# Optimization experiments

Measured on AMD Instinct MI355X. Metric: run time of the kernel, lower is better.

Reference implementation:

```python
import jax, jax.numpy as jnp
import numpy as np

GFD = 4096   # global feature dim (VGG fc7)
DH = 1024    # 2 * hidden_dim


def setup_inputs() -> dict:
    key = jax.random.key(0)
    ks = jax.random.split(key, 10)
    b, t_k = 32, 196
    s = lambda fan_in: 1.0 / np.sqrt(fan_in)
    return {
        "global_features": jax.random.normal(ks[0], (b, t_k, GFD), jnp.float32),
        "s_t_hat": jax.random.normal(ks[1], (b, DH), jnp.float32),
        "coverage_img": jnp.zeros((b, t_k, 1), jnp.float32),
        # params
        "Wg": jax.random.normal(ks[2], (GFD, GFD), jnp.float32) * s(GFD),
        "bg": jnp.zeros((GFD,), jnp.float32),
        "Gs": jax.random.normal(ks[3], (GFD, DH), jnp.float32) * s(GFD),
        "bgs": jnp.zeros((DH,), jnp.float32),
        "Wgs": jax.random.normal(ks[4], (DH, DH), jnp.float32) * s(DH),  # w_g_star, no bias
        "Wdec": jax.random.normal(ks[5], (DH, DH), jnp.float32) * s(DH),  # decode_proj
        "bdec": jnp.zeros((DH,), jnp.float32),
        "v": jax.random.normal(ks[6], (DH, 1), jnp.float32) * s(DH),  # score vector, no bias
    }


def reference(global_features, s_t_hat, coverage_img, Wg, bg, Gs, bgs, Wgs, Wdec, bdec, v):
    # g_star: project 4096-d region features -> 1024-d   [b, t_k, DH]
    g1 = global_features @ Wg + bg
    g_star = g1 @ Gs + bgs
    # additive (Bahdanau) scores with coverage
    w_g_star = g_star @ Wgs                       # [b, t_k, DH]
    dec_fea = s_t_hat @ Wdec + bdec               # [b, DH]
    e_a = jnp.tanh(w_g_star + dec_fea[:, None, :] + coverage_img)  # [b, t_k, DH]
    scores = e_a @ v                              # [b, t_k, 1]
    alpha_a = jax.nn.softmax(scores, axis=1)      # softmax over regions
    # attention-weighted context (the bmm)
    c_img = jnp.einsum("bt,btd->bd", alpha_a[..., 0], g_star)  # [b, DH]
    coverage_new = coverage_img + alpha_a
    return c_img, coverage_new, alpha_a
```

## Files before the change

### kernel.cpp

```cpp
#include <hip/hip_runtime.h>
#include <hip/hip_bf16.h>

typedef __attribute__((ext_vector_type(8))) short short8;
typedef __attribute__((ext_vector_type(4))) short short4v;
typedef __attribute__((ext_vector_type(4))) float floatx4;

#define GLOBAL_AS __attribute__((address_space(1)))
#define LDS_AS    __attribute__((address_space(3)))

__device__ __forceinline__ unsigned short f2bf_rne(float x) {
  unsigned int u = __float_as_uint(x);
  u += 0x7fffu + ((u >> 16) & 1u);
  return (unsigned short)(u >> 16);
}

__device__ __forceinline__ void cast8_body(const float* __restrict__ in,
                                           unsigned short* __restrict__ out,
                                           int blk, int n8) {
  int i = blk * 256 + threadIdx.x;
  if (i >= n8) return;
  const float4* p = (const float4*)in;
  float4 v0 = p[2 * i], v1 = p[2 * i + 1];
  short8 o;
  o[0] = (short)f2bf_rne(v0.x); o[1] = (short)f2bf_rne(v0.y);
  o[2] = (short)f2bf_rne(v0.z); o[3] = (short)f2bf_rne(v0.w);
  o[4] = (short)f2bf_rne(v1.x); o[5] = (short)f2bf_rne(v1.y);
  o[6] = (short)f2bf_rne(v1.z); o[7] = (short)f2bf_rne(v1.w);
  *(short8*)(out + 8 * (size_t)i) = o;
}

__device__ __forceinline__ void trans32_body(const float* __restrict__ in,
                                             unsigned short* __restrict__ out,
                                             int R, int C, int bx, int by) {
  __shared__ unsigned short tile[32][33];
  int tx = threadIdx.x & 31, ty = threadIdx.x >> 5;
  int r0 = by * 32, c0 = bx * 32;
#pragma unroll
  for (int j = 0; j < 32; j += 8)
    tile[ty + j][tx] = f2bf_rne(in[(size_t)(r0 + ty + j) * C + c0 + tx]);
  __syncthreads();
#pragma unroll
  for (int j = 0; j < 32; j += 8)
    out[(size_t)(c0 + ty + j) * R + r0 + tx] = tile[tx][ty + j];
}

__global__ void prep1_kernel(const float* __restrict__ gf, unsigned short* __restrict__ gf_bf,
                             const float* __restrict__ Wg, unsigned short* __restrict__ Wg_bf,
                             const float* __restrict__ Gs, unsigned short* __restrict__ GsT,
                             const float* __restrict__ bg, float* __restrict__ bias1,
                             const float* __restrict__ Wgs, unsigned short* __restrict__ WgsT,
                             const float* __restrict__ bdec, float* __restrict__ dec,
                             float* __restrict__ scores) {
  const int b = blockIdx.x;
  if (b < 12544) {
    cast8_body(gf, gf_bf, b, 3211264);
  } else if (b < 20736) {
    cast8_body(Wg, Wg_bf, b - 12544, 2097152);
  } else if (b < 24832) {
    int bb = b - 20736;
    trans32_body(Gs, GsT, 4096, 1024, bb & 31, bb >> 5);
  } else if (b < 24896) {
    int bb = b - 24832;
    int j = (bb & 3) * 256 + threadIdx.x;
    int k0 = (bb >> 2) * 256;
    float acc = 0.f;
    for (int k = 0; k < 256; ++k) acc += bg[k0 + k] * Gs[(size_t)(k0 + k) * 1024 + j];
    atomicAdd(&bias1[j], acc);
  } else if (b < 25920) {
    int bb = b - 24896;
    trans32_body(Wgs, WgsT, 1024, 1024, bb & 31, bb >> 5);
  } else if (b < 26048) {
    int i = (b - 25920) * 256 + threadIdx.x;
    dec[i] = bdec[i & 1023];
  } else {
    int i = (b - 26048) * 256 + threadIdx.x;
    if (i < 1568) ((float4*)scores)[i] = make_float4(0.f, 0.f, 0.f, 0.f);
  }
}

__global__ void dec_accum_kernel(const float* __restrict__ sth, const float* __restrict__ Wdec,
                                 float* __restrict__ dec) {
  __shared__ float ss[32][128];
  const int tid = threadIdx.x;
  const int k0 = blockIdx.y * 128;
  for (int i = tid; i < 32 * 128; i += 256) {
    int bb = i >> 7, kk = i & 127;
    ss[bb][kk] = sth[bb * 1024 + k0 + kk];
  }
  __syncthreads();
  const int j = blockIdx.x * 256 + tid;
  float acc[32];
#pragma unroll
  for (int b = 0; b < 32; ++b) acc[b] = 0.f;
  for (int kk = 0; kk < 128; ++kk) {
    float w = Wdec[(size_t)(k0 + kk) * 1024 + j];
#pragma unroll
    for (int b = 0; b < 32; ++b) acc[b] += ss[b][kk] * w;
  }
  for (int b = 0; b < 32; ++b) atomicAdd(&dec[b * 1024 + j], acc[b]);
}

__global__ __launch_bounds__(256) void reduce2_kernel(const float* __restrict__ p0,
                                                      const float* __restrict__ p1,
                                                      const float* __restrict__ bias,
                                                      float* __restrict__ gf32,
                                                      unsigned short* __restrict__ gb16) {
  const int i = blockIdx.x * 256 + threadIdx.x;
  float4 a = ((const float4*)p0)[i];
  float4 b = ((const float4*)p1)[i];
  float4 bv = ((const float4*)bias)[i & 255];
  float4 r;
  r.x = a.x + b.x + bv.x; r.y = a.y + b.y + bv.y;
  r.z = a.z + b.z + bv.z; r.w = a.w + b.w + bv.w;
  ((float4*)gf32)[i] = r;
  short4v o;
  o[0] = (short)f2bf_rne(r.x); o[1] = (short)f2bf_rne(r.y);
  o[2] = (short)f2bf_rne(r.z); o[3] = (short)f2bf_rne(r.w);
  *(short4v*)(gb16 + 4 * (size_t)i) = o;
}

template <int BM, int BN, bool WRITE_F32, bool WRITE_BF16, bool SWAPXY>
__global__ __launch_bounds__(256, 2) void gemm_tile_kernel(
    const unsigned short* __restrict__ A, const unsigned short* __restrict__ BT,
    float* __restrict__ Cf, unsigned short* __restrict__ Cb,
    int M, int N, int K, int Ksub, size_t csplit) {
  constexpr int AF = BM / 32;
  constexpr int BF = BN / 32;
  constexpr int ASLAB = BM * 64;
  constexpr int BSLAB = BN * 64;
  constexpr int ABUF = 2 * ASLAB;
  constexpr int BBUF = 2 * BSLAB;
  __shared__ unsigned short lds_a[BM * 128];
  __shared__ unsigned short lds_b[BN * 128];
  const int tid = threadIdx.x;
  const int lane = tid & 63;
  const int wave = tid >> 6;
  const int wm = wave >> 1, wn = wave & 1;
  const int quad = lane >> 4, col = lane & 15;

  const int gx = (int)gridDim.x;
  const int nwg = gx * (int)gridDim.y;
  const int bid = (int)blockIdx.y * gx + (int)blockIdx.x;
  const int swz = (bid & 7) * (nwg >> 3) + (bid >> 3);
  const int bx = swz % gx, by = swz / gx;
  const int m0 = (SWAPXY ? bx : by) * BM;
  const int n0 = (SWAPXY ? by : bx) * BN;
  const int kb = (int)blockIdx.z * Ksub;

  floatx4 acc[AF][BF] = {};

  const int srow = tid >> 2;
  const int skoff = (tid & 3) * 8;
  const unsigned short* a_ptr = A + (size_t)(m0 + srow) * K + kb + skoff;
  const unsigned short* b_ptr = BT + (size_t)(n0 + srow) * K + kb + skoff;
  const size_t rowskip = (size_t)64 * K;
  char* const la_dst = (char*)lds_a + tid * 16;
  char* const lb_dst = (char*)lds_b + tid * 16;

#pragma unroll
  for (int h = 0; h < BM / 64; ++h)
#pragma unroll
    for (int s = 0; s < 2; ++s)
      __builtin_amdgcn_global_load_lds((const GLOBAL_AS void*)(a_ptr + h * rowskip + s * 32),
                                       (LDS_AS void*)(la_dst + s * ASLAB + h * 4096), 16, 0, 0);
#pragma unroll
  for (int h = 0; h < BN / 64; ++h)
#pragma unroll
    for (int s = 0; s < 2; ++s)
      __builtin_amdgcn_global_load_lds((const GLOBAL_AS void*)(b_ptr + h * rowskip + s * 32),
                                       (LDS_AS void*)(lb_dst + s * BSLAB + h * 4096), 16, 0, 0);
  a_ptr += 64; b_ptr += 64;
  __syncthreads();

  const int NT = Ksub >> 6;
  int cur = 0;
  for (int t = 0; t < NT; ++t) {
    if (t + 1 < NT) {
      char* la = la_dst + (cur ^ 1) * ABUF;
      char* lb = lb_dst + (cur ^ 1) * BBUF;
#pragma unroll
      for (int h = 0; h < BM / 64; ++h)
#pragma unroll
        for (int s = 0; s < 2; ++s)
          __builtin_amdgcn_global_load_lds((const GLOBAL_AS void*)(a_ptr + h * rowskip + s * 32),
                                           (LDS_AS void*)(la + s * ASLAB + h * 4096), 16, 0, 0);
#pragma unroll
      for (int h = 0; h < BN / 64; ++h)
#pragma unroll
        for (int s = 0; s < 2; ++s)
          __builtin_amdgcn_global_load_lds((const GLOBAL_AS void*)(b_ptr + h * rowskip + s * 32),
                                           (LDS_AS void*)(lb + s * BSLAB + h * 4096), 16, 0, 0);
      a_ptr += 64; b_ptr += 64;
    }
    const char* pa = (const char*)lds_a + cur * ABUF;
    const char* pb = (const char*)lds_b + cur * BBUF;
#pragma unroll
    for (int s = 0; s < 2; ++s) {
      short8 af[AF], bf[BF];
#pragma unroll
      for (int tf = 0; tf < AF; ++tf)
        af[tf] = *(const short8*)(pa + s * ASLAB + (wm * (BM / 2) + tf * 16 + col) * 64 + quad * 16);
#pragma unroll
      for (int tf = 0; tf < BF; ++tf)
        bf[tf] = *(const short8*)(pb + s * BSLAB + (wn * (BN / 2) + tf * 16 + col) * 64 + quad * 16);
#pragma unroll
      for (int tm = 0; tm < AF; ++tm)
#pragma unroll
        for (int tn = 0; tn < BF; ++tn)
          acc[tm][tn] = __builtin_amdgcn_mfma_f32_16x16x32_bf16(af[tm], bf[tn], acc[tm][tn], 0, 0, 0);
    }
    __syncthreads();
    cur ^= 1;
  }

  float* Cfz = Cf + (size_t)blockIdx.z * csplit;
#pragma unroll
  for (int tm = 0; tm < AF; ++tm) {
    const int mg = m0 + wm * (BM / 2) + tm * 16 + quad * 4;
#pragma unroll
    for (int tn = 0; tn < BF; ++tn) {
      const int ng = n0 + wn * (BN / 2) + tn * 16 + col;
#pragma unroll
      for (int r = 0; r < 4; ++r) {
        const float val = acc[tm][tn][r];
        if (WRITE_F32) Cfz[(size_t)(mg + r) * N + ng] = val;
        if (WRITE_BF16) Cb[(size_t)(mg + r) * N + ng] = f2bf_rne(val);
      }
    }
  }
}

__global__ __launch_bounds__(256, 2) void gemm_scores_kernel(
    const unsigned short* __restrict__ A, const unsigned short* __restrict__ BT,
    const float* __restrict__ dec, const float* __restrict__ cov,
    const float* __restrict__ v, float* __restrict__ scores, int M, int N, int K) {
  constexpr int ASLAB = 8192, ABUF = 16384;
  constexpr int BSLAB = 4096, BBUF = 8192;
  __shared__ unsigned short lds_a[128 * 128];
  __shared__ unsigned short lds_b[64 * 128];
  const int tid = threadIdx.x;
  const int lane = tid & 63;
  const int wave = tid >> 6;
  const int wm = wave >> 1, wn = wave & 1;
  const int quad = lane >> 4, col = lane & 15;

  const int gx = (int)gridDim.x;
  const int nwg = gx * (int)gridDim.y;
  const int bid = (int)blockIdx.y * gx + (int)blockIdx.x;
  const int swz = (bid & 7) * (nwg >> 3) + (bid >> 3);
  const int m0 = (swz / gx) * 128, n0 = (swz % gx) * 64;

  floatx4 acc[4][2] = {};

  const int srow = tid >> 2;
  const int skoff = (tid & 3) * 8;
  const unsigned short* a_ptr = A + (size_t)(m0 + srow) * K + skoff;
  const unsigned short* b_ptr = BT + (size_t)(n0 + srow) * K + skoff;
  const size_t rowskip = (size_t)64 * K;
  char* const la_dst = (char*)lds_a + tid * 16;
  char* const lb_dst = (char*)lds_b + tid * 16;

#pragma unroll
  for (int h = 0; h < 2; ++h)
#pragma unroll
    for (int s = 0; s < 2; ++s)
      __builtin_amdgcn_global_load_lds((const GLOBAL_AS void*)(a_ptr + h * rowskip + s * 32),
                                       (LDS_AS void*)(la_dst + s * ASLAB + h * 4096), 16, 0, 0);
#pragma unroll
  for (int s = 0; s < 2; ++s)
    __builtin_amdgcn_global_load_lds((const GLOBAL_AS void*)(b_ptr + s * 32),
                                     (LDS_AS void*)(lb_dst + s * BSLAB), 16, 0, 0);
  a_ptr += 64; b_ptr += 64;
  __syncthreads();

  const int NT = K >> 6;
  int cur = 0;
  for (int t = 0; t < NT; ++t) {
    if (t + 1 < NT) {
      char* la = la_dst + (cur ^ 1) * ABUF;
      char* lb = lb_dst + (cur ^ 1) * BBUF;
#pragma unroll
      for (int h = 0; h < 2; ++h)
#pragma unroll
        for (int s = 0; s < 2; ++s)
          __builtin_amdgcn_global_load_lds((const GLOBAL_AS void*)(a_ptr + h * rowskip + s * 32),
                                           (LDS_AS void*)(la + s * ASLAB + h * 4096), 16, 0, 0);
#pragma unroll
      for (int s = 0; s < 2; ++s)
        __builtin_amdgcn_global_load_lds((const GLOBAL_AS void*)(b_ptr + s * 32),
                                         (LDS_AS void*)(lb + s * BSLAB), 16, 0, 0);
      a_ptr += 64; b_ptr += 64;
    }
    const char* pa = (const char*)lds_a + cur * ABUF;
    const char* pb = (const char*)lds_b + cur * BBUF;
#pragma unroll
    for (int s = 0; s < 2; ++s) {
      short8 af[4], bf[2];
#pragma unroll
      for (int tf = 0; tf < 4; ++tf)
        af[tf] = *(const short8*)(pa + s * ASLAB + (wm * 64 + tf * 16 + col) * 64 + quad * 16);
#pragma unroll
      for (int tf = 0; tf < 2; ++tf)
        bf[tf] = *(const short8*)(pb + s * BSLAB + (wn * 32 + tf * 16 + col) * 64 + quad * 16);
#pragma unroll
      for (int tm = 0; tm < 4; ++tm)
#pragma unroll
        for (int tn = 0; tn < 2; ++tn)
          acc[tm][tn] = __builtin_amdgcn_mfma_f32_16x16x32_bf16(af[tm], bf[tn], acc[tm][tn], 0, 0, 0);
    }
    __syncthreads();
    cur ^= 1;
  }

  const int n_base = n0 + wn * 32;
  float vv[2];
#pragma unroll
  for (int tn = 0; tn < 2; ++tn) vv[tn] = v[n_base + tn * 16 + col];
#pragma unroll
  for (int tm = 0; tm < 4; ++tm) {
#pragma unroll
    for (int r = 0; r < 4; ++r) {
      const int row = m0 + wm * 64 + tm * 16 + quad * 4 + r;
      const int b = row / 196;
      const float cw = cov[row];
      const float* dr = dec + b * 1024 + n_base;
      float s = 0.f;
#pragma unroll
      for (int tn = 0; tn < 2; ++tn)
        s += tanhf(acc[tm][tn][r] + dr[tn * 16 + col] + cw) * vv[tn];
      s += __shfl_xor(s, 1, 64);
      s += __shfl_xor(s, 2, 64);
      s += __shfl_xor(s, 4, 64);
      s += __shfl_xor(s, 8, 64);
      if ((lane & 15) == 0) atomicAdd(&scores[row], s);
    }
  }
}

__global__ void softmax_kernel(const float* __restrict__ scores, const float* __restrict__ cov,
                               float* __restrict__ alpha_ws, float* __restrict__ out) {
  const int b = blockIdx.x, tid = threadIdx.x;
  const int lane = tid & 63, wid = tid >> 6;
  __shared__ float red[8];
  float s = (tid < 196) ? scores[b * 196 + tid] : -1e30f;
  float m = s;
  for (int off = 32; off > 0; off >>= 1) m = fmaxf(m, __shfl_xor(m, off, 64));
  if (lane == 0) red[wid] = m;
  __syncthreads();
  m = fmaxf(fmaxf(red[0], red[1]), fmaxf(red[2], red[3]));
  float e = (tid < 196) ? __expf(s - m) : 0.f;
  float t = e;
  for (int off = 32; off > 0; off >>= 1) t += __shfl_xor(t, off, 64);
  if (lane == 0) red[4 + wid] = t;
  __syncthreads();
  const float tot = red[4] + red[5] + red[6] + red[7];
  const float a = e / tot;
  if (tid < 196) {
    alpha_ws[b * 196 + tid] = a;
    out[32768 + b * 196 + tid] = cov[b * 196 + tid] + a;
    out[32768 + 6272 + b * 196 + tid] = a;
  }
}

__global__ __launch_bounds__(256) void ctx_kernel(const float* __restrict__ alpha,
                                                  const float* __restrict__ gstar,
                                                  float* __restrict__ out) {
  const int b = blockIdx.y;
  const int colbase = blockIdx.x * 128;
  const int c = threadIdx.x & 127;
  const int half = threadIdx.x >> 7;
  const float* g = gstar + ((size_t)b * 196 + half * 98) * 1024 + colbase + c;
  const float* al = alpha + b * 196 + half * 98;
  float acc = 0.f;
#pragma unroll 7
  for (int t = 0; t < 98; ++t) acc += al[t] * g[(size_t)t * 1024];
  __shared__ float part[256];
  part[threadIdx.x] = acc;
  __syncthreads();
  if (threadIdx.x < 128)
    out[b * 1024 + colbase + threadIdx.x] = part[threadIdx.x] + part[threadIdx.x + 128];
}

extern "C" void kernel_launch(void* const* d_in, const int* in_sizes, int n_in,
                              void* d_out, int out_size, void* d_ws, size_t ws_size,
                              hipStream_t stream) {
  (void)in_sizes; (void)n_in; (void)out_size; (void)ws_size;
  const float* gf   = (const float*)d_in[0];
  const float* sth  = (const float*)d_in[1];
  const float* cov  = (const float*)d_in[2];
  const float* Wg   = (const float*)d_in[3];
  const float* bg   = (const float*)d_in[4];
  const float* Gs   = (const float*)d_in[5];
  const float* bgs  = (const float*)d_in[6];
  const float* Wgs  = (const float*)d_in[7];
  const float* Wdec = (const float*)d_in[8];
  const float* bdec = (const float*)d_in[9];
  const float* v    = (const float*)d_in[10];
  float* out = (float*)d_out;

  char* ws = (char*)d_ws;
  unsigned short* gf_bf   = (unsigned short*)(ws + 0);
  unsigned short* gstar_b = (unsigned short*)(ws + 0);
  unsigned short* Wg_bf   = (unsigned short*)(ws + 51380224);
  float*          p0      = (float*)(ws + 51380224);
  float*          gstar_f = (float*)(ws + 51380224);
  float*          p1      = (float*)(ws + 77070336);
  unsigned short* GsT     = (unsigned short*)(ws + 84934656);
  unsigned short* C1T_b   = (unsigned short*)(ws + 102760448);
  unsigned short* WgsT    = (unsigned short*)(ws + 111149056);
  float*          bias1   = (float*)(ws + 113246208);
  float*          dec     = (float*)(ws + 113262592);
  float*          scores  = (float*)(ws + 113393664);
  float*          alpha   = (float*)(ws + 113426432);

  hipMemcpyAsync(bias1, bgs, 4096, hipMemcpyDeviceToDevice, stream);
  prep1_kernel<<<26055, 256, 0, stream>>>(gf, gf_bf, Wg, Wg_bf, Gs, GsT, bg, bias1,
                                          Wgs, WgsT, bdec, dec, scores);
  dec_accum_kernel<<<dim3(4, 8), 256, 0, stream>>>(sth, Wdec, dec);
  gemm_tile_kernel<128, 64, false, true, true><<<dim3(8, 64, 1), 256, 0, stream>>>(
      GsT, Wg_bf, nullptr, C1T_b, 1024, 4096, 4096, 4096, 0);
  gemm_tile_kernel<128, 128, true, false, false><<<dim3(8, 49, 2), 256, 0, stream>>>(
      gf_bf, C1T_b, p0, nullptr, 6272, 1024, 4096, 2048, 6422528);
  reduce2_kernel<<<6272, 256, 0, stream>>>(p0, p1, bias1, gstar_f, gstar_b);
  gemm_scores_kernel<<<dim3(16, 49), 256, 0, stream>>>(
      gstar_b, WgsT, dec, cov, v, scores, 6272, 1024, 1024);
  softmax_kernel<<<32, 256, 0, stream>>>(scores, cov, alpha, out);
  ctx_kernel<<<dim3(8, 32), 256, 0, stream>>>(alpha, gstar_f, out);
}
```

Measured before the change: 518.5 us.

## Drop split-K and fuse bias/bf16 epilogue into GEMM; XOR-swizzle LDS layout

Removes the split-K=2 path for the large g_star GEMM, so the reduce kernel that summed partials, added the bias and cast to bf16 is gone. Bias add plus fp32 and bf16 stores now happen in the GEMM epilogue. This avoids writing and re-reading two fp32 partial buffers at the cost of fewer workgroups (392 instead of 784), which lowers occupancy and K-parallelism. It also applies an XOR swizzle to the LDS column chunks in both GEMM kernels to cut bank conflicts on the fragment reads.

```diff
diff --git a/kernel.cpp b/kernel.cpp
--- a/kernel.cpp
+++ b/kernel.cpp
@@ -2,7 +2,6 @@
 #include <hip/hip_bf16.h>
 
 typedef __attribute__((ext_vector_type(8))) short short8;
-typedef __attribute__((ext_vector_type(4))) short short4v;
 typedef __attribute__((ext_vector_type(4))) float floatx4;
 
 #define GLOBAL_AS __attribute__((address_space(1)))
@@ -100,30 +99,11 @@
   for (int b = 0; b < 32; ++b) atomicAdd(&dec[b * 1024 + j], acc[b]);
 }
 
-__global__ __launch_bounds__(256) void reduce2_kernel(const float* __restrict__ p0,
-                                                      const float* __restrict__ p1,
-                                                      const float* __restrict__ bias,
-                                                      float* __restrict__ gf32,
-                                                      unsigned short* __restrict__ gb16) {
-  const int i = blockIdx.x * 256 + threadIdx.x;
-  float4 a = ((const float4*)p0)[i];
-  float4 b = ((const float4*)p1)[i];
-  float4 bv = ((const float4*)bias)[i & 255];
-  float4 r;
-  r.x = a.x + b.x + bv.x; r.y = a.y + b.y + bv.y;
-  r.z = a.z + b.z + bv.z; r.w = a.w + b.w + bv.w;
-  ((float4*)gf32)[i] = r;
-  short4v o;
-  o[0] = (short)f2bf_rne(r.x); o[1] = (short)f2bf_rne(r.y);
-  o[2] = (short)f2bf_rne(r.z); o[3] = (short)f2bf_rne(r.w);
-  *(short4v*)(gb16 + 4 * (size_t)i) = o;
-}
-
-template <int BM, int BN, bool WRITE_F32, bool WRITE_BF16, bool SWAPXY>
+template <int BM, int BN, bool HAS_BIAS, bool WRITE_F32, bool WRITE_BF16, bool SWAPXY>
 __global__ __launch_bounds__(256, 2) void gemm_tile_kernel(
     const unsigned short* __restrict__ A, const unsigned short* __restrict__ BT,
-    float* __restrict__ Cf, unsigned short* __restrict__ Cb,
-    int M, int N, int K, int Ksub, size_t csplit) {
+    const float* __restrict__ bias, float* __restrict__ Cf,
+    unsigned short* __restrict__ Cb, int M, int N, int K) {
   constexpr int AF = BM / 32;
   constexpr int BF = BN / 32;
   constexpr int ASLAB = BM * 64;
@@ -145,17 +125,17 @@
   const int bx = swz % gx, by = swz / gx;
   const int m0 = (SWAPXY ? bx : by) * BM;
   const int n0 = (SWAPXY ? by : bx) * BN;
-  const int kb = (int)blockIdx.z * Ksub;
 
   floatx4 acc[AF][BF] = {};
 
   const int srow = tid >> 2;
-  const int skoff = (tid & 3) * 8;
-  const unsigned short* a_ptr = A + (size_t)(m0 + srow) * K + kb + skoff;
-  const unsigned short* b_ptr = BT + (size_t)(n0 + srow) * K + kb + skoff;
+  const int skoff = ((tid & 3) ^ ((tid >> 3) & 3)) * 8;
+  const unsigned short* a_ptr = A + (size_t)(m0 + srow) * K + skoff;
+  const unsigned short* b_ptr = BT + (size_t)(n0 + srow) * K + skoff;
   const size_t rowskip = (size_t)64 * K;
   char* const la_dst = (char*)lds_a + tid * 16;
   char* const lb_dst = (char*)lds_b + tid * 16;
+  const int cx = (quad ^ ((col >> 1) & 3)) * 16;
 
 #pragma unroll
   for (int h = 0; h < BM / 64; ++h)
@@ -172,7 +152,7 @@
   a_ptr += 64; b_ptr += 64;
   __syncthreads();
 
-  const int NT = Ksub >> 6;
+  const int NT = K >> 6;
   int cur = 0;
   for (int t = 0; t < NT; ++t) {
     if (t + 1 < NT) {
@@ -199,10 +179,10 @@
       short8 af[AF], bf[BF];
 #pragma unroll
       for (int tf = 0; tf < AF; ++tf)
-        af[tf] = *(const short8*)(pa + s * ASLAB + (wm * (BM / 2) + tf * 16 + col) * 64 + quad * 16);
+        af[tf] = *(const short8*)(pa + s * ASLAB + (wm * (BM / 2) + tf * 16 + col) * 64 + cx);
 #pragma unroll
       for (int tf = 0; tf < BF; ++tf)
-        bf[tf] = *(const short8*)(pb + s * BSLAB + (wn * (BN / 2) + tf * 16 + col) * 64 + quad * 16);
+        bf[tf] = *(const short8*)(pb + s * BSLAB + (wn * (BN / 2) + tf * 16 + col) * 64 + cx);
 #pragma unroll
       for (int tm = 0; tm < AF; ++tm)
 #pragma unroll
@@ -213,17 +193,17 @@
     cur ^= 1;
   }
 
-  float* Cfz = Cf + (size_t)blockIdx.z * csplit;
 #pragma unroll
   for (int tm = 0; tm < AF; ++tm) {
     const int mg = m0 + wm * (BM / 2) + tm * 16 + quad * 4;
 #pragma unroll
     for (int tn = 0; tn < BF; ++tn) {
       const int ng = n0 + wn * (BN / 2) + tn * 16 + col;
+      const float bv = HAS_BIAS ? bias[ng] : 0.0f;
 #pragma unroll
       for (int r = 0; r < 4; ++r) {
-        const float val = acc[tm][tn][r];
-        if (WRITE_F32) Cfz[(size_t)(mg + r) * N + ng] = val;
+        const float val = acc[tm][tn][r] + bv;
+        if (WRITE_F32) Cf[(size_t)(mg + r) * N + ng] = val;
         if (WRITE_BF16) Cb[(size_t)(mg + r) * N + ng] = f2bf_rne(val);
       }
     }
@@ -253,12 +233,13 @@
   floatx4 acc[4][2] = {};
 
   const int srow = tid >> 2;
-  const int skoff = (tid & 3) * 8;
+  const int skoff = ((tid & 3) ^ ((tid >> 3) & 3)) * 8;
   const unsigned short* a_ptr = A + (size_t)(m0 + srow) * K + skoff;
   const unsigned short* b_ptr = BT + (size_t)(n0 + srow) * K + skoff;
   const size_t rowskip = (size_t)64 * K;
   char* const la_dst = (char*)lds_a + tid * 16;
   char* const lb_dst = (char*)lds_b + tid * 16;
+  const int cx = (quad ^ ((col >> 1) & 3)) * 16;
 
 #pragma unroll
   for (int h = 0; h < 2; ++h)
@@ -298,10 +279,10 @@
       short8 af[4], bf[2];
 #pragma unroll
       for (int tf = 0; tf < 4; ++tf)
-        af[tf] = *(const short8*)(pa + s * ASLAB + (wm * 64 + tf * 16 + col) * 64 + quad * 16);
+        af[tf] = *(const short8*)(pa + s * ASLAB + (wm * 64 + tf * 16 + col) * 64 + cx);
 #pragma unroll
       for (int tf = 0; tf < 2; ++tf)
-        bf[tf] = *(const short8*)(pb + s * BSLAB + (wn * 32 + tf * 16 + col) * 64 + quad * 16);
+        bf[tf] = *(const short8*)(pb + s * BSLAB + (wn * 32 + tf * 16 + col) * 64 + cx);
 #pragma unroll
       for (int tm = 0; tm < 4; ++tm)
 #pragma unroll
@@ -400,12 +381,10 @@
 
   char* ws = (char*)d_ws;
   unsigned short* gf_bf   = (unsigned short*)(ws + 0);
-  unsigned short* gstar_b = (unsigned short*)(ws + 0);
   unsigned short* Wg_bf   = (unsigned short*)(ws + 51380224);
-  float*          p0      = (float*)(ws + 51380224);
   float*          gstar_f = (float*)(ws + 51380224);
-  float*          p1      = (float*)(ws + 77070336);
   unsigned short* GsT     = (unsigned short*)(ws + 84934656);
+  unsigned short* gstar_b = (unsigned short*)(ws + 84934656);
   unsigned short* C1T_b   = (unsigned short*)(ws + 102760448);
   unsigned short* WgsT    = (unsigned short*)(ws + 111149056);
   float*          bias1   = (float*)(ws + 113246208);
@@ -417,11 +396,10 @@
   prep1_kernel<<<26055, 256, 0, stream>>>(gf, gf_bf, Wg, Wg_bf, Gs, GsT, bg, bias1,
                                           Wgs, WgsT, bdec, dec, scores);
   dec_accum_kernel<<<dim3(4, 8), 256, 0, stream>>>(sth, Wdec, dec);
-  gemm_tile_kernel<128, 64, false, true, true><<<dim3(8, 64, 1), 256, 0, stream>>>(
-      GsT, Wg_bf, nullptr, C1T_b, 1024, 4096, 4096, 4096, 0);
-  gemm_tile_kernel<128, 128, true, false, false><<<dim3(8, 49, 2), 256, 0, stream>>>(
-      gf_bf, C1T_b, p0, nullptr, 6272, 1024, 4096, 2048, 6422528);
-  reduce2_kernel<<<6272, 256, 0, stream>>>(p0, p1, bias1, gstar_f, gstar_b);
+  gemm_tile_kernel<128, 64, false, false, true, true><<<dim3(8, 64), 256, 0, stream>>>(
+      GsT, Wg_bf, nullptr, nullptr, C1T_b, 1024, 4096, 4096);
+  gemm_tile_kernel<128, 128, true, true, true, false><<<dim3(8, 49), 256, 0, stream>>>(
+      gf_bf, C1T_b, bias1, gstar_f, gstar_b, 6272, 1024, 4096);
   gemm_scores_kernel<<<dim3(16, 49), 256, 0, stream>>>(
       gstar_b, WgsT, dec, cov, v, scores, 6272, 1024, 1024);
   softmax_kernel<<<32, 256, 0, stream>>>(scores, cov, alpha, out);
```

Measured after the change: 487.1 us. 1.06x faster.
